# Kernel optimization log

Measured on AMD Instinct MI355X. Metric: run time of the kernel, lower is better.

Reference implementation:

```python
import jax, jax.numpy as jnp
import numpy as np

N, H, S, R, T = 32768, 512, 8, 64, 12

def setup_inputs() -> dict:
    key = jax.random.key(0)
    ks = jax.random.split(key, 7)
    scale = 1.0 / np.sqrt(H)
    return {
        "encodings": jax.random.normal(ks[0], (N, H), dtype=jnp.float32),
        "domain_encs": jax.random.normal(ks[1], (S, H), dtype=jnp.float32),
        "Us": jax.random.normal(ks[2], (S, H, R), dtype=jnp.float32) * scale,
        "W1": jax.random.normal(ks[3], (S, H, H), dtype=jnp.float32) * scale,
        "b1": jax.random.normal(ks[4], (S, H), dtype=jnp.float32) * 0.01,
        "W2": jax.random.normal(ks[5], (S, H, T), dtype=jnp.float32) * scale,
        "b2": jax.random.normal(ks[6], (S, T), dtype=jnp.float32) * 0.01,
    }

def reference(encodings, domain_encs, Us, W1, b1, W2, b2):
    # Mahalanobis soft routing. Original computes (p-mu) @ (U U^T) @ (p-mu)^T
    # and takes sqrt(diag) -- algebraically identical to project-then-square-sum.
    diff = encodings[None, :, :] - domain_encs[:, None, :]        # [S, N, H]
    proj = jnp.einsum('snh,shr->snr', diff, Us)                   # [S, N, R]
    dist = jnp.sqrt(jnp.sum(proj * proj, axis=-1))                # [S, N]
    alphas = jax.nn.softmax(-dist, axis=0)                        # softmax over sources

    # Per-source classifier: Dropout(eval=identity) -> ReLU -> Linear(H,H)
    # -> Dropout -> ReLU -> Linear(H,T) -> Sigmoid
    h0 = jax.nn.relu(encodings)                                   # [N, H]
    h1 = jax.nn.relu(jnp.einsum('nh,shk->snk', h0, W1) + b1[:, None, :])  # [S, N, H]
    out = jax.nn.sigmoid(jnp.einsum('snk,skt->snt', h1, W2) + b2[:, None, :])  # [S, N, T]

    # Softmax-weighted combine of expert outputs
    return jnp.sum(alphas[:, :, None] * out, axis=0)              # [N, T]
```

## Files before the change

kernel.cpp:

```cpp
#include <hip/hip_runtime.h>
#include <hip/hip_bf16.h>

typedef unsigned short u16;
typedef __bf16 bf16x8 __attribute__((ext_vector_type(8)));
typedef float f32x4 __attribute__((ext_vector_type(4)));

#define NROWS 32768
#define H 512
#define NS 8
#define NR 64
#define NT 12

#define WS_W1T   0
#define WS_UCT   4194304
#define WS_W2T   4718592
#define WS_CVEC  4849664
#define WS_ALPH  4851712

union BFU { __bf16 h; u16 u; };
__device__ __forceinline__ u16 f2bf(float v) { BFU b; b.h = (__bf16)v; return b.u; }

__device__ __forceinline__ void gload16(const u16* g, u16* l) {
  __builtin_amdgcn_global_load_lds(
      (const __attribute__((address_space(1))) unsigned int*)g,
      (__attribute__((address_space(3))) unsigned int*)l, 16, 0, 0);
}

__global__ __launch_bounds__(256) void transpose_cast(const float* __restrict__ in,
    u16* __restrict__ out, int Rr, int Cc, int Cpad) {
  __shared__ float tile[32][33];
  int b = blockIdx.z, r0 = blockIdx.x * 32, c0 = blockIdx.y * 32;
  int tx = threadIdx.x, ty = threadIdx.y;
#pragma unroll
  for (int i = 0; i < 4; i++) {
    int r = r0 + ty + i * 8, c = c0 + tx;
    float v = 0.f;
    if (r < Rr && c < Cc) v = in[((size_t)b * Rr + r) * Cc + c];
    tile[ty + i * 8][tx] = v;
  }
  __syncthreads();
#pragma unroll
  for (int i = 0; i < 4; i++) {
    int c = c0 + ty + i * 8, r = r0 + tx;
    if (c < Cpad && r < Rr) out[((size_t)b * Cpad + c) * Rr + r] = f2bf(tile[tx][ty + i * 8]);
  }
}

__global__ __launch_bounds__(64) void compute_c(const float* __restrict__ mu,
                                                const float* __restrict__ Us,
                                                float* __restrict__ cvec) {
  int s = blockIdx.x >> 6, r = blockIdx.x & 63, t = threadIdx.x;
  float acc = 0.f;
#pragma unroll
  for (int k = t; k < H; k += 64) acc += mu[s * H + k] * Us[((size_t)s * H + k) * NR + r];
#pragma unroll
  for (int m = 32; m; m >>= 1) acc += __shfl_xor(acc, m, 64);
  if (t == 0) cvec[blockIdx.x] = acc;
}

__device__ __forceinline__ void stage32r(const u16* __restrict__ g, u16* l, int wave, int lane) {
#pragma unroll
  for (int i = 0; i < 8; i++) {
    int r = wave * 8 + i;
    gload16(g + (size_t)r * 512 + (size_t)((lane ^ (r & 7)) * 8), l + r * 512);
  }
}

__global__ __launch_bounds__(256, 2) void routing(
    const float* __restrict__ enc, const u16* __restrict__ UcatT,
    const float* __restrict__ cvec, float* __restrict__ alphT) {
  __shared__ __align__(16) u16 Wst[2][32 * 512];
  __shared__ float distS[NS][64];

  const int tid = threadIdx.x;
  const int wave = tid >> 6, lane = tid & 63;
  const int lnm = lane & 15, lnq = lane >> 4;
  const int row0 = blockIdx.x * 64;

  bf16x8 afrag[16];
  {
    const float* rp = enc + (size_t)(row0 + wave * 16 + lnm) * H + lnq * 8;
#pragma unroll
    for (int ks = 0; ks < 16; ks++) {
      float4 x0 = *(const float4*)(rp + ks * 32);
      float4 x1 = *(const float4*)(rp + ks * 32 + 4);
      bf16x8 a;
      a[0] = (__bf16)x0.x; a[1] = (__bf16)x0.y; a[2] = (__bf16)x0.z; a[3] = (__bf16)x0.w;
      a[4] = (__bf16)x1.x; a[5] = (__bf16)x1.y; a[6] = (__bf16)x1.z; a[7] = (__bf16)x1.w;
      afrag[ks] = a;
    }
  }

  stage32r(UcatT, Wst[0], wave, lane);
  float dsq[4] = {0.f, 0.f, 0.f, 0.f};
#pragma unroll 1
  for (int q = 0; q < 16; q++) {
    int s = q >> 1, half = q & 1;
    __syncthreads();
    if (q < 15) stage32r(UcatT + (size_t)(q + 1) * 32 * 512, Wst[(q + 1) & 1], wave, lane);
    const u16* buf = Wst[q & 1];
    f32x4 acc[2] = {};
#pragma unroll
    for (int ks = 0; ks < 16; ks++) {
      int uu = ((ks * 4 + lnq) ^ (lnm & 7)) * 8;
      bf16x8 b0 = *(const bf16x8*)&buf[lnm * 512 + uu];
      bf16x8 b1v = *(const bf16x8*)&buf[(16 + lnm) * 512 + uu];
      acc[0] = __builtin_amdgcn_mfma_f32_16x16x32_bf16(afrag[ks], b0, acc[0], 0, 0, 0);
      acc[1] = __builtin_amdgcn_mfma_f32_16x16x32_bf16(afrag[ks], b1v, acc[1], 0, 0, 0);
    }
#pragma unroll
    for (int ct = 0; ct < 2; ct++) {
      float cv = cvec[s * 64 + half * 32 + ct * 16 + lnm];
#pragma unroll
      for (int g = 0; g < 4; g++) { float d = acc[ct][g] - cv; dsq[g] += d * d; }
    }
    if (half == 1) {
#pragma unroll
      for (int m = 1; m < 16; m <<= 1) {
#pragma unroll
        for (int g = 0; g < 4; g++) dsq[g] += __shfl_xor(dsq[g], m, 16);
      }
      if (lnm == 0) {
#pragma unroll
        for (int g = 0; g < 4; g++) distS[s][wave * 16 + lnq * 4 + g] = sqrtf(dsq[g]);
      }
#pragma unroll
      for (int g = 0; g < 4; g++) dsq[g] = 0.f;
    }
  }
  __syncthreads();
  if (tid < 64) {
    float dmin = distS[0][tid];
#pragma unroll
    for (int s = 1; s < NS; s++) dmin = fminf(dmin, distS[s][tid]);
    float den = 0.f, e[NS];
#pragma unroll
    for (int s = 0; s < NS; s++) { e[s] = __expf(dmin - distS[s][tid]); den += e[s]; }
    float inv = 1.f / den;
#pragma unroll
    for (int s = 0; s < NS; s++) alphT[(size_t)s * NROWS + row0 + tid] = e[s] * inv;
  }
}

#define H1STR 40

__device__ __forceinline__ void stageW16(const u16* __restrict__ g, u16* l, int tid) {
#pragma unroll
  for (int i = 0; i < 4; i++) {
    int flat = tid + i * 256;
    int r = flat >> 5, u = flat & 31;
    gload16(g + (size_t)r * 512 + (u ^ (r & 7)) * 8, l + flat * 8);
  }
}

__device__ __forceinline__ const u16* chunk_base(const u16* W1g, int q) {
  return W1g + ((size_t)(q >> 5) * 512 + ((q >> 1) & 15) * 32) * 512 + (q & 1) * 256;
}

__global__ __launch_bounds__(256, 2) void moe_main(
    const float* __restrict__ enc, const u16* __restrict__ W1T,
    const u16* __restrict__ W2T, const float* __restrict__ alphT,
    const float* __restrict__ b1g, const float* __restrict__ b2g,
    float* __restrict__ out) {
  __shared__ __align__(16) u16 Wst[2][32 * 256];
  __shared__ __align__(16) u16 h1c[128 * H1STR];
  __shared__ float alphS[4][128];

  const int tid = threadIdx.x;
  const int wave = tid >> 6, lane = tid & 63;
  const int lnm = lane & 15, lnq = lane >> 4;
  const int rb = blockIdx.x >> 1, sg = blockIdx.x & 1;
  const int row0 = rb * 128, sbase = sg * 4;

#pragma unroll
  for (int i = 0; i < 2; i++) {
    int u = tid + i * 256, j = u >> 7, r = u & 127;
    alphS[j][r] = alphT[(size_t)(sbase + j) * NROWS + row0 + r];
  }

  bf16x8 efrag[2][16];
#pragma unroll
  for (int t = 0; t < 2; t++) {
    const float* rp = enc + (size_t)(row0 + wave * 32 + t * 16 + lnm) * H + lnq * 8;
#pragma unroll
    for (int ks = 0; ks < 16; ks++) {
      float4 x0 = *(const float4*)(rp + ks * 32);
      float4 x1 = *(const float4*)(rp + ks * 32 + 4);
      bf16x8 a;
      a[0] = (__bf16)fmaxf(x0.x, 0.f); a[1] = (__bf16)fmaxf(x0.y, 0.f);
      a[2] = (__bf16)fmaxf(x0.z, 0.f); a[3] = (__bf16)fmaxf(x0.w, 0.f);
      a[4] = (__bf16)fmaxf(x1.x, 0.f); a[5] = (__bf16)fmaxf(x1.y, 0.f);
      a[6] = (__bf16)fmaxf(x1.z, 0.f); a[7] = (__bf16)fmaxf(x1.w, 0.f);
      efrag[t][ks] = a;
    }
  }

  const u16* W1g = W1T + (size_t)sbase * 512 * 512;
  stageW16(chunk_base(W1g, 0), Wst[0], tid);
  f32x4 acc[2][2];
  float fin[2][4] = {};
#pragma unroll 1
  for (int j = 0; j < 4; j++) {
    const int s = sbase + j;
    f32x4 oacc[2] = {};
#pragma unroll 1
    for (int wc = 0; wc < 16; wc++) {
      const int q = j * 32 + wc * 2;
      __syncthreads();
      stageW16(chunk_base(W1g, q + 1), Wst[1], tid);
      {
        const u16* buf = Wst[0];
#pragma unroll
        for (int t = 0; t < 2; t++) { acc[t][0] = (f32x4){0,0,0,0}; acc[t][1] = (f32x4){0,0,0,0}; }
#pragma unroll
        for (int ks = 0; ks < 8; ks++) {
          const int uu = ((ks * 4 + lnq) ^ (lnm & 7)) * 8;
          bf16x8 w0 = *(const bf16x8*)&buf[lnm * 256 + uu];
          bf16x8 w1 = *(const bf16x8*)&buf[(16 + lnm) * 256 + uu];
#pragma unroll
          for (int t = 0; t < 2; t++) {
            acc[t][0] = __builtin_amdgcn_mfma_f32_16x16x32_bf16(w0, efrag[t][ks], acc[t][0], 0, 0, 0);
            acc[t][1] = __builtin_amdgcn_mfma_f32_16x16x32_bf16(w1, efrag[t][ks], acc[t][1], 0, 0, 0);
          }
        }
      }
      __syncthreads();
      if (q + 2 < 128) stageW16(chunk_base(W1g, q + 2), Wst[0], tid);
      {
        const u16* buf = Wst[1];
#pragma unroll
        for (int ks = 0; ks < 8; ks++) {
          const int uu = ((ks * 4 + lnq) ^ (lnm & 7)) * 8;
          bf16x8 w0 = *(const bf16x8*)&buf[lnm * 256 + uu];
          bf16x8 w1 = *(const bf16x8*)&buf[(16 + lnm) * 256 + uu];
#pragma unroll
          for (int t = 0; t < 2; t++) {
            acc[t][0] = __builtin_amdgcn_mfma_f32_16x16x32_bf16(w0, efrag[t][8 + ks], acc[t][0], 0, 0, 0);
            acc[t][1] = __builtin_amdgcn_mfma_f32_16x16x32_bf16(w1, efrag[t][8 + ks], acc[t][1], 0, 0, 0);
          }
        }
      }
#pragma unroll
      for (int ct = 0; ct < 2; ct++) {
        float4 bq = *(const float4*)&b1g[s * H + wc * 32 + ct * 16 + lnq * 4];
#pragma unroll
        for (int t = 0; t < 2; t++) {
          union { u16 u[4]; uint2 v; } pk;
          pk.u[0] = f2bf(fmaxf(acc[t][ct][0] + bq.x, 0.f));
          pk.u[1] = f2bf(fmaxf(acc[t][ct][1] + bq.y, 0.f));
          pk.u[2] = f2bf(fmaxf(acc[t][ct][2] + bq.z, 0.f));
          pk.u[3] = f2bf(fmaxf(acc[t][ct][3] + bq.w, 0.f));
          *(uint2*)&h1c[(wave * 32 + t * 16 + lnm) * H1STR + ct * 16 + lnq * 4] = pk.v;
        }
      }
      {
        bf16x8 bw = *(const bf16x8*)&W2T[((size_t)s * 16 + lnm) * H + wc * 32 + lnq * 8];
#pragma unroll
        for (int t = 0; t < 2; t++) {
          bf16x8 a2 = *(const bf16x8*)&h1c[(wave * 32 + t * 16 + lnm) * H1STR + lnq * 8];
          oacc[t] = __builtin_amdgcn_mfma_f32_16x16x32_bf16(a2, bw, oacc[t], 0, 0, 0);
        }
      }
    }
    {
      float b2v = (lnm < NT) ? b2g[s * NT + lnm] : 0.f;
#pragma unroll
      for (int t = 0; t < 2; t++) {
#pragma unroll
        for (int g = 0; g < 4; g++) {
          float sig = 1.f / (1.f + __expf(-(oacc[t][g] + b2v)));
          fin[t][g] += alphS[j][wave * 32 + t * 16 + lnq * 4 + g] * sig;
        }
      }
    }
  }
  if (lnm < NT) {
#pragma unroll
    for (int t = 0; t < 2; t++) {
#pragma unroll
      for (int g = 0; g < 4; g++) {
        int rg = row0 + wave * 32 + t * 16 + lnq * 4 + g;
        atomicAdd(&out[(size_t)rg * NT + lnm], fin[t][g]);
      }
    }
  }
}

extern "C" void kernel_launch(void* const* d_in, const int* in_sizes, int n_in,
                              void* d_out, int out_size, void* d_ws, size_t ws_size,
                              hipStream_t stream) {
  const float* enc = (const float*)d_in[0];
  const float* mu  = (const float*)d_in[1];
  const float* Us  = (const float*)d_in[2];
  const float* W1  = (const float*)d_in[3];
  const float* b1  = (const float*)d_in[4];
  const float* W2  = (const float*)d_in[5];
  const float* b2  = (const float*)d_in[6];
  float* out = (float*)d_out;
  char* ws = (char*)d_ws;
  u16* W1T    = (u16*)(ws + WS_W1T);
  u16* UcatT  = (u16*)(ws + WS_UCT);
  u16* W2T    = (u16*)(ws + WS_W2T);
  float* cvec = (float*)(ws + WS_CVEC);
  float* alphT = (float*)(ws + WS_ALPH);

  dim3 tb(32, 8, 1);
  transpose_cast<<<dim3(16, 16, 8), tb, 0, stream>>>(W1, W1T, 512, 512, 512);
  transpose_cast<<<dim3(16, 2, 8),  tb, 0, stream>>>(Us, UcatT, 512, 64, 64);
  transpose_cast<<<dim3(16, 1, 8),  tb, 0, stream>>>(W2, W2T, 512, 12, 16);
  compute_c<<<512, 64, 0, stream>>>(mu, Us, cvec);
  routing<<<512, 256, 0, stream>>>(enc, UcatT, cvec, alphT);
  hipMemsetAsync(out, 0, (size_t)out_size * sizeof(float), stream);
  moe_main<<<512, 256, 0, stream>>>(enc, W1T, W2T, alphT, b1, b2, out);
}
```

Baseline: 300.4 us.

## Split MoE sources into four groups, fuse transposes, widen LDS swizzle

moe_main now runs 1024 blocks, each handling 2 sources instead of 4. This doubles the block count so more CUs stay busy, at the cost of loading the encoding fragments and accumulating into the output twice as often. The three weight transpose/cast launches are merged into one kernel dispatched over a z-range, which removes launch overhead. The LDS XOR swizzle is widened from 8 to 16 lanes in both the staging writes and the fragment reads, to reduce bank conflicts.

```diff
diff --git a/kernel.cpp b/kernel.cpp
--- a/kernel.cpp
+++ b/kernel.cpp
@@ -26,23 +26,42 @@
       (__attribute__((address_space(3))) unsigned int*)l, 16, 0, 0);
 }
 
-__global__ __launch_bounds__(256) void transpose_cast(const float* __restrict__ in,
-    u16* __restrict__ out, int Rr, int Cc, int Cpad) {
-  __shared__ float tile[32][33];
-  int b = blockIdx.z, r0 = blockIdx.x * 32, c0 = blockIdx.y * 32;
-  int tx = threadIdx.x, ty = threadIdx.y;
+__device__ __forceinline__ void tile_transpose(const float* __restrict__ in,
+    u16* __restrict__ out, int Rr, int Cc, int Cpad, int r0, int c0,
+    int tx, int ty, float (*tile)[33]) {
 #pragma unroll
   for (int i = 0; i < 4; i++) {
     int r = r0 + ty + i * 8, c = c0 + tx;
     float v = 0.f;
-    if (r < Rr && c < Cc) v = in[((size_t)b * Rr + r) * Cc + c];
+    if (r < Rr && c < Cc) v = in[(size_t)r * Cc + c];
     tile[ty + i * 8][tx] = v;
   }
   __syncthreads();
 #pragma unroll
   for (int i = 0; i < 4; i++) {
     int c = c0 + ty + i * 8, r = r0 + tx;
-    if (c < Cpad && r < Rr) out[((size_t)b * Cpad + c) * Rr + r] = f2bf(tile[tx][ty + i * 8]);
+    if (c < Cpad && r < Rr) out[(size_t)c * Rr + r] = f2bf(tile[tx][ty + i * 8]);
+  }
+}
+
+__global__ __launch_bounds__(256) void fused_transpose(
+    const float* __restrict__ W1, u16* __restrict__ W1T,
+    const float* __restrict__ Us, u16* __restrict__ UcT,
+    const float* __restrict__ W2, u16* __restrict__ W2T) {
+  __shared__ float tile[32][33];
+  int tx = threadIdx.x, ty = threadIdx.y, z = blockIdx.z;
+  if (z < 8) {
+    tile_transpose(W1 + (size_t)z * 512 * 512, W1T + (size_t)z * 512 * 512,
+                   512, 512, 512, blockIdx.x * 32, blockIdx.y * 32, tx, ty, tile);
+  } else if (z == 8) {
+    int b = blockIdx.y >> 1, c0 = (blockIdx.y & 1) * 32;
+    tile_transpose(Us + (size_t)b * 512 * 64, UcT + (size_t)b * 64 * 512,
+                   512, 64, 64, blockIdx.x * 32, c0, tx, ty, tile);
+  } else {
+    if (blockIdx.y >= 8) return;
+    int b = blockIdx.y;
+    tile_transpose(W2 + (size_t)b * 512 * 12, W2T + (size_t)b * 16 * 512,
+                   512, 12, 16, blockIdx.x * 32, 0, tx, ty, tile);
   }
 }
 
@@ -62,7 +81,7 @@
 #pragma unroll
   for (int i = 0; i < 8; i++) {
     int r = wave * 8 + i;
-    gload16(g + (size_t)r * 512 + (size_t)((lane ^ (r & 7)) * 8), l + r * 512);
+    gload16(g + (size_t)r * 512 + (size_t)((lane ^ (r & 15)) * 8), l + r * 512);
   }
 }
 
@@ -102,7 +121,7 @@
     f32x4 acc[2] = {};
 #pragma unroll
     for (int ks = 0; ks < 16; ks++) {
-      int uu = ((ks * 4 + lnq) ^ (lnm & 7)) * 8;
+      int uu = ((ks * 4 + lnq) ^ (lnm & 15)) * 8;
       bf16x8 b0 = *(const bf16x8*)&buf[lnm * 512 + uu];
       bf16x8 b1v = *(const bf16x8*)&buf[(16 + lnm) * 512 + uu];
       acc[0] = __builtin_amdgcn_mfma_f32_16x16x32_bf16(afrag[ks], b0, acc[0], 0, 0, 0);
@@ -149,7 +168,7 @@
   for (int i = 0; i < 4; i++) {
     int flat = tid + i * 256;
     int r = flat >> 5, u = flat & 31;
-    gload16(g + (size_t)r * 512 + (u ^ (r & 7)) * 8, l + flat * 8);
+    gload16(g + (size_t)r * 512 + (u ^ (r & 15)) * 8, l + flat * 8);
   }
 }
 
@@ -164,19 +183,16 @@
     float* __restrict__ out) {
   __shared__ __align__(16) u16 Wst[2][32 * 256];
   __shared__ __align__(16) u16 h1c[128 * H1STR];
-  __shared__ float alphS[4][128];
+  __shared__ float alphS[2][128];
 
   const int tid = threadIdx.x;
   const int wave = tid >> 6, lane = tid & 63;
   const int lnm = lane & 15, lnq = lane >> 4;
-  const int rb = blockIdx.x >> 1, sg = blockIdx.x & 1;
-  const int row0 = rb * 128, sbase = sg * 4;
-
-#pragma unroll
-  for (int i = 0; i < 2; i++) {
-    int u = tid + i * 256, j = u >> 7, r = u & 127;
-    alphS[j][r] = alphT[(size_t)(sbase + j) * NROWS + row0 + r];
-  }
+  const int rb = blockIdx.x >> 2, sg = blockIdx.x & 3;
+  const int row0 = rb * 128, sbase = sg * 2;
+
+  { int j = tid >> 7, r = tid & 127;
+    alphS[j][r] = alphT[(size_t)(sbase + j) * NROWS + row0 + r]; }
 
   bf16x8 efrag[2][16];
 #pragma unroll
@@ -200,7 +216,7 @@
   f32x4 acc[2][2];
   float fin[2][4] = {};
 #pragma unroll 1
-  for (int j = 0; j < 4; j++) {
+  for (int j = 0; j < 2; j++) {
     const int s = sbase + j;
     f32x4 oacc[2] = {};
 #pragma unroll 1
@@ -214,7 +230,7 @@
         for (int t = 0; t < 2; t++) { acc[t][0] = (f32x4){0,0,0,0}; acc[t][1] = (f32x4){0,0,0,0}; }
 #pragma unroll
         for (int ks = 0; ks < 8; ks++) {
-          const int uu = ((ks * 4 + lnq) ^ (lnm & 7)) * 8;
+          const int uu = ((ks * 4 + lnq) ^ (lnm & 15)) * 8;
           bf16x8 w0 = *(const bf16x8*)&buf[lnm * 256 + uu];
           bf16x8 w1 = *(const bf16x8*)&buf[(16 + lnm) * 256 + uu];
 #pragma unroll
@@ -225,12 +241,12 @@
         }
       }
       __syncthreads();
-      if (q + 2 < 128) stageW16(chunk_base(W1g, q + 2), Wst[0], tid);
+      if (q + 2 < 64) stageW16(chunk_base(W1g, q + 2), Wst[0], tid);
       {
         const u16* buf = Wst[1];
 #pragma unroll
         for (int ks = 0; ks < 8; ks++) {
-          const int uu = ((ks * 4 + lnq) ^ (lnm & 7)) * 8;
+          const int uu = ((ks * 4 + lnq) ^ (lnm & 15)) * 8;
           bf16x8 w0 = *(const bf16x8*)&buf[lnm * 256 + uu];
           bf16x8 w1 = *(const bf16x8*)&buf[(16 + lnm) * 256 + uu];
 #pragma unroll
@@ -305,11 +321,9 @@
   float* alphT = (float*)(ws + WS_ALPH);
 
   dim3 tb(32, 8, 1);
-  transpose_cast<<<dim3(16, 16, 8), tb, 0, stream>>>(W1, W1T, 512, 512, 512);
-  transpose_cast<<<dim3(16, 2, 8),  tb, 0, stream>>>(Us, UcatT, 512, 64, 64);
-  transpose_cast<<<dim3(16, 1, 8),  tb, 0, stream>>>(W2, W2T, 512, 12, 16);
+  fused_transpose<<<dim3(16, 16, 10), tb, 0, stream>>>(W1, W1T, Us, UcatT, W2, W2T);
   compute_c<<<512, 64, 0, stream>>>(mu, Us, cvec);
   routing<<<512, 256, 0, stream>>>(enc, UcatT, cvec, alphT);
   hipMemsetAsync(out, 0, (size_t)out_size * sizeof(float), stream);
-  moe_main<<<512, 256, 0, stream>>>(enc, W1T, W2T, alphT, b1, b2, out);
-}
+  moe_main<<<1024, 256, 0, stream>>>(enc, W1T, W2T, alphT, b1, b2, out);
+}
```

New measurement: 333.2 us. 1.11x slower.
